# Optimization experiments

Hardware: AMD Instinct MI355X
Metric: run time of the kernel (lower is better)

The kernel has to match this reference:

```python
import jax, jax.numpy as jnp
import numpy as np

QUERY_SIZE = 512
KEY_SIZE = 512
VALUE_SIZE = 512
HIDDEN = 128


def setup_inputs() -> dict:
    key = jax.random.key(0)
    ks = jax.random.split(key, 9)
    b, t_q, t_k = 8, 128, 512
    query = jax.random.normal(ks[0], (b, t_q, QUERY_SIZE), dtype=jnp.float32)
    keys = jax.random.normal(ks[1], (b, t_k, KEY_SIZE), dtype=jnp.float32)
    values = jax.random.normal(ks[2], (b, t_k, VALUE_SIZE), dtype=jnp.float32)
    # torch nn.Linear init ~ U(-1/sqrt(fan_in), 1/sqrt(fan_in)); scale-matched normals are fine
    sq = 1.0 / np.sqrt(QUERY_SIZE)
    sk = 1.0 / np.sqrt(KEY_SIZE)
    sh = 1.0 / np.sqrt(HIDDEN)
    Wq = jax.random.uniform(ks[3], (HIDDEN, QUERY_SIZE), jnp.float32, -sq, sq)
    bq = jax.random.uniform(ks[4], (HIDDEN,), jnp.float32, -sq, sq)
    Wk = jax.random.uniform(ks[5], (HIDDEN, KEY_SIZE), jnp.float32, -sk, sk)
    bk = jax.random.uniform(ks[6], (HIDDEN,), jnp.float32, -sk, sk)
    Wo = jax.random.uniform(ks[7], (1, HIDDEN), jnp.float32, -sh, sh)
    bo = jax.random.uniform(ks[8], (1,), jnp.float32, -sh, sh)
    return {"query": query, "keys": keys, "values": values,
            "Wq": Wq, "bq": bq, "Wk": Wk, "bk": bk, "Wo": Wo, "bo": bo}


def reference(query, keys, values, Wq, bq, Wk, bk, Wo, bo):
    # Bahdanau additive attention: att_ij = Wo @ tanh(Wq q_i + Wk k_j + bq + bk) + bo
    # Project once per position (mathematically identical to the expanded per-pair Linear).
    q_proj = jnp.einsum('bqn,hn->bqh', query, Wq) + bq          # b x t_q x h
    k_proj = jnp.einsum('bkn,hn->bkh', keys, Wk) + bk           # b x t_k x h
    hid = jnp.tanh(q_proj[:, :, None, :] + k_proj[:, None, :, :])  # b x t_q x t_k x h
    scores = jnp.einsum('bqkh,h->bqk', hid, Wo[0]) + bo[0]       # b x t_q x t_k
    attn = jax.nn.softmax(scores, axis=2)
    context = jnp.einsum('bqk,bkv->bqv', attn, values)           # b x t_q x n_v
    return context, attn
```

## Files before the change

### kernel.cpp

```cpp
#include <hip/hip_runtime.h>


#define B_    8
#define TQ_   128
#define TK_   512
#define NIN_  512
#define H_    128
#define NV_   512
#define NQR   (B_*TQ_)
#define NROWS (NQR + B_*TK_)

#define C2_   2.8853900817779268f
#define L2E_  1.4426950408889634f

__device__ __forceinline__ float fexp2(float x){ return __builtin_amdgcn_exp2f(x); }
__device__ __forceinline__ float frcp (float x){ return __builtin_amdgcn_rcpf(x); }

__global__ __launch_bounds__(256, 5) void proj_kernel(
        const float* __restrict__ query, const float* __restrict__ keys,
        const float* __restrict__ Wq, const float* __restrict__ Wk,
        float* __restrict__ psum, int kper) {
    __shared__ float at[32][18];
    __shared__ float wt[32][132];
    const int tid = threadIdx.x;
    const int r0  = blockIdx.x * 16;
    const float* in; const float* W;
    if (r0 < NQR) { in = query + (size_t)r0 * NIN_;         W = Wq; }
    else          { in = keys  + (size_t)(r0 - NQR) * NIN_; W = Wk; }

    const int r2 = (tid >> 5) * 2;
    const int h4 = (tid & 31) * 4;
    const int ar  = tid >> 4;
    const int ak2 = (tid & 15) * 2;
    const int wr  = tid >> 3;
    const int wkq = (tid & 7) * 4;
    const int kb0 = blockIdx.y * kper;
    const int nc  = kper >> 5;

    const float* pA  = in + ar * NIN_ + kb0 + ak2;
    const float* pW0 = W + (wr     ) * NIN_ + kb0 + wkq;
    const float* pW1 = W + (wr + 32) * NIN_ + kb0 + wkq;
    const float* pW2 = W + (wr + 64) * NIN_ + kb0 + wkq;
    const float* pW3 = W + (wr + 96) * NIN_ + kb0 + wkq;

    float2 af  = *(const float2*)pA;
    float4 wf0 = *(const float4*)pW0;
    float4 wf1 = *(const float4*)pW1;
    float4 wf2 = *(const float4*)pW2;
    float4 wf3 = *(const float4*)pW3;

    float acc[2][4] = {{0.f,0.f,0.f,0.f},{0.f,0.f,0.f,0.f}};

    for (int c = 0; c < nc; ++c) {
        __syncthreads();
        at[ak2+0][ar] = af.x;  at[ak2+1][ar] = af.y;
        wt[wkq+0][wr   ] = wf0.x; wt[wkq+1][wr   ] = wf0.y;
        wt[wkq+2][wr   ] = wf0.z; wt[wkq+3][wr   ] = wf0.w;
        wt[wkq+0][wr+32] = wf1.x; wt[wkq+1][wr+32] = wf1.y;
        wt[wkq+2][wr+32] = wf1.z; wt[wkq+3][wr+32] = wf1.w;
        wt[wkq+0][wr+64] = wf2.x; wt[wkq+1][wr+64] = wf2.y;
        wt[wkq+2][wr+64] = wf2.z; wt[wkq+3][wr+64] = wf2.w;
        wt[wkq+0][wr+96] = wf3.x; wt[wkq+1][wr+96] = wf3.y;
        wt[wkq+2][wr+96] = wf3.z; wt[wkq+3][wr+96] = wf3.w;
        __syncthreads();
        if (c + 1 < nc) {
            pA += 32; pW0 += 32; pW1 += 32; pW2 += 32; pW3 += 32;
            af  = *(const float2*)pA;
            wf0 = *(const float4*)pW0; wf1 = *(const float4*)pW1;
            wf2 = *(const float4*)pW2; wf3 = *(const float4*)pW3;
        }
#pragma unroll 8
        for (int kk = 0; kk < 32; ++kk) {
            float2 a = *(const float2*)&at[kk][r2];
            float4 w = *(const float4*)&wt[kk][h4];
            acc[0][0] = fmaf(a.x, w.x, acc[0][0]);
            acc[0][1] = fmaf(a.x, w.y, acc[0][1]);
            acc[0][2] = fmaf(a.x, w.z, acc[0][2]);
            acc[0][3] = fmaf(a.x, w.w, acc[0][3]);
            acc[1][0] = fmaf(a.y, w.x, acc[1][0]);
            acc[1][1] = fmaf(a.y, w.y, acc[1][1]);
            acc[1][2] = fmaf(a.y, w.z, acc[1][2]);
            acc[1][3] = fmaf(a.y, w.w, acc[1][3]);
        }
    }

    float* op = psum + ((size_t)blockIdx.y * NROWS + r0) * H_;
#pragma unroll
    for (int i = 0; i < 2; ++i) {
        float4 o = {acc[i][0], acc[i][1], acc[i][2], acc[i][3]};
        *(float4*)&op[(r2 + i) * H_ + h4] = o;
    }
}

__global__ __launch_bounds__(256, 4) void reduce_kernel(
        const float* __restrict__ psum, const float* __restrict__ bq,
        const float* __restrict__ bk, float* __restrict__ pout) {
    const int i = blockIdx.x * 256 + threadIdx.x;
    const int row = i >> 5;
    const int h4  = (i & 31) * 4;
    const float* bias = (row < NQR) ? bq : bk;
    float4 s = *(const float4*)&bias[h4];
#pragma unroll
    for (int sp = 0; sp < 4; ++sp) {
        float4 p = *(const float4*)&psum[((size_t)sp * NROWS) * H_ + (size_t)i * 4];
        s.x += p.x; s.y += p.y; s.z += p.z; s.w += p.w;
    }
    *(float4*)&pout[(size_t)i * 4] = s;
}

__global__ __launch_bounds__(256, 4) void scores_kernel(
        const float* __restrict__ qp, const float* __restrict__ kp,
        const float* __restrict__ Wo, const float* __restrict__ bo,
        float* __restrict__ out_attn) {
    __shared__ float qs2[2][H_];
    __shared__ float w2[H_];
    __shared__ float sc[2][TK_];

    const int tid = threadIdx.x;
    const int b   = blockIdx.y;
    const int q0  = blockIdx.x * 2;
    const int lane = tid & 63;

    qs2[tid >> 7][tid & 127] =
        qp[(b * TQ_ + q0 + (tid >> 7)) * H_ + (tid & 127)] * C2_;
    if (tid < H_) w2[tid] = Wo[tid] * -2.0f;
    __syncthreads();

    float sw = w2[lane] + w2[lane + 64];
#pragma unroll
    for (int m = 1; m < 64; m <<= 1) sw += __shfl_xor(sw, m);
    const float sbase = bo[0] - 0.5f * sw;

#pragma unroll
    for (int half = 0; half < 2; ++half) {
        const int k = tid + half * 256;
        const float4* kp4 = (const float4*)&kp[(b * TK_ + k) * H_];
        float acc[2] = {0.f, 0.f};
#pragma unroll 4
        for (int hb = 0; hb < 32; ++hb) {
            float4 kv = kp4[hb];
            kv.x *= C2_; kv.y *= C2_; kv.z *= C2_; kv.w *= C2_;
            float4 wv = *(const float4*)&w2[hb * 4];
#pragma unroll
            for (int qi = 0; qi < 2; ++qi) {
                float4 qv = *(const float4*)&qs2[qi][hb * 4];
                float r0 = frcp(fexp2(qv.x + kv.x) + 1.0f);
                float r1 = frcp(fexp2(qv.y + kv.y) + 1.0f);
                float r2 = frcp(fexp2(qv.z + kv.z) + 1.0f);
                float r3 = frcp(fexp2(qv.w + kv.w) + 1.0f);
                acc[qi] = fmaf(wv.x, r0, acc[qi]);
                acc[qi] = fmaf(wv.y, r1, acc[qi]);
                acc[qi] = fmaf(wv.z, r2, acc[qi]);
                acc[qi] = fmaf(wv.w, r3, acc[qi]);
            }
        }
        sc[0][k] = acc[0] + sbase;
        sc[1][k] = acc[1] + sbase;
    }
    __syncthreads();

    const int w = tid >> 6;
    if (w < 2) {
        float4 sA = *(const float4*)&sc[w][lane * 8];
        float4 sB = *(const float4*)&sc[w][lane * 8 + 4];
        float m = fmaxf(fmaxf(fmaxf(sA.x, sA.y), fmaxf(sA.z, sA.w)),
                        fmaxf(fmaxf(sB.x, sB.y), fmaxf(sB.z, sB.w)));
#pragma unroll
        for (int mask = 1; mask < 64; mask <<= 1) m = fmaxf(m, __shfl_xor(m, mask));
        float4 eA, eB;
        eA.x = fexp2((sA.x - m) * L2E_); eA.y = fexp2((sA.y - m) * L2E_);
        eA.z = fexp2((sA.z - m) * L2E_); eA.w = fexp2((sA.w - m) * L2E_);
        eB.x = fexp2((sB.x - m) * L2E_); eB.y = fexp2((sB.y - m) * L2E_);
        eB.z = fexp2((sB.z - m) * L2E_); eB.w = fexp2((sB.w - m) * L2E_);
        float s = eA.x + eA.y + eA.z + eA.w + eB.x + eB.y + eB.z + eB.w;
#pragma unroll
        for (int mask = 1; mask < 64; mask <<= 1) s += __shfl_xor(s, mask);
        float inv = frcp(s);
        eA.x *= inv; eA.y *= inv; eA.z *= inv; eA.w *= inv;
        eB.x *= inv; eB.y *= inv; eB.z *= inv; eB.w *= inv;
        float4* op = (float4*)&out_attn[(b * TQ_ + q0 + w) * TK_ + lane * 8];
        op[0] = eA; op[1] = eB;
    }
}

__global__ __launch_bounds__(256, 4) void context_kernel(
        const float* __restrict__ attn, const float* __restrict__ values,
        float* __restrict__ outc) {
    __shared__ float at[32][20];
    __shared__ float vt[32][132];

    const int tid = threadIdx.x;
    const int b   = blockIdx.y;
    const int q0  = (blockIdx.x >> 2) * 16;
    const int v0  = (blockIdx.x & 3) * 128;

    const int tx = tid & 31, ty = tid >> 5;
    const int v4 = tx * 4,   r2 = ty * 2;
    const int ar = tid >> 3, akq = (tid & 7) * 4;
    const int vk = tid >> 5;

    const float* pAt = attn + (size_t)(b * TQ_ + q0 + ar) * TK_ + akq;
    const float* pV0 = values + (size_t)(b * TK_ + vk     ) * NV_ + v0 + v4;
    const float* pV1 = values + (size_t)(b * TK_ + vk +  8) * NV_ + v0 + v4;
    const float* pV2 = values + (size_t)(b * TK_ + vk + 16) * NV_ + v0 + v4;
    const float* pV3 = values + (size_t)(b * TK_ + vk + 24) * NV_ + v0 + v4;

    float4 af = {0.f,0.f,0.f,0.f};
    if (tid < 128) af = *(const float4*)pAt;
    float4 vf0 = *(const float4*)pV0;
    float4 vf1 = *(const float4*)pV1;
    float4 vf2 = *(const float4*)pV2;
    float4 vf3 = *(const float4*)pV3;

    float acc[2][4] = {{0.f,0.f,0.f,0.f},{0.f,0.f,0.f,0.f}};

    for (int c = 0; c < 16; ++c) {
        __syncthreads();
        if (tid < 128) {
            at[akq+0][ar] = af.x; at[akq+1][ar] = af.y;
            at[akq+2][ar] = af.z; at[akq+3][ar] = af.w;
        }
        *(float4*)&vt[vk     ][v4] = vf0;
        *(float4*)&vt[vk +  8][v4] = vf1;
        *(float4*)&vt[vk + 16][v4] = vf2;
        *(float4*)&vt[vk + 24][v4] = vf3;
        __syncthreads();
        if (c + 1 < 16) {
            pAt += 32; pV0 += 32 * NV_; pV1 += 32 * NV_;
            pV2 += 32 * NV_; pV3 += 32 * NV_;
            if (tid < 128) af = *(const float4*)pAt;
            vf0 = *(const float4*)pV0; vf1 = *(const float4*)pV1;
            vf2 = *(const float4*)pV2; vf3 = *(const float4*)pV3;
        }
#pragma unroll 8
        for (int kk = 0; kk < 32; ++kk) {
            float2 a = *(const float2*)&at[kk][r2];
            float4 v = *(const float4*)&vt[kk][v4];
            acc[0][0] = fmaf(a.x, v.x, acc[0][0]);
            acc[0][1] = fmaf(a.x, v.y, acc[0][1]);
            acc[0][2] = fmaf(a.x, v.z, acc[0][2]);
            acc[0][3] = fmaf(a.x, v.w, acc[0][3]);
            acc[1][0] = fmaf(a.y, v.x, acc[1][0]);
            acc[1][1] = fmaf(a.y, v.y, acc[1][1]);
            acc[1][2] = fmaf(a.y, v.z, acc[1][2]);
            acc[1][3] = fmaf(a.y, v.w, acc[1][3]);
        }
    }
    float4 o0 = {acc[0][0], acc[0][1], acc[0][2], acc[0][3]};
    float4 o1 = {acc[1][0], acc[1][1], acc[1][2], acc[1][3]};
    *(float4*)&outc[(size_t)(b * TQ_ + q0 + r2 + 0) * NV_ + v0 + v4] = o0;
    *(float4*)&outc[(size_t)(b * TQ_ + q0 + r2 + 1) * NV_ + v0 + v4] = o1;
}

extern "C" void kernel_launch(void* const* d_in, const int* in_sizes, int n_in,
                              void* d_out, int out_size, void* d_ws, size_t ws_size,
                              hipStream_t stream) {
    const float* query  = (const float*)d_in[0];
    const float* keys   = (const float*)d_in[1];
    const float* values = (const float*)d_in[2];
    const float* Wq     = (const float*)d_in[3];
    const float* bq     = (const float*)d_in[4];
    const float* Wk     = (const float*)d_in[5];
    const float* bk     = (const float*)d_in[6];
    const float* Wo     = (const float*)d_in[7];
    const float* bo     = (const float*)d_in[8];

    float* out_ctx  = (float*)d_out;
    float* out_attn = out_ctx + B_ * TQ_ * NV_;
    float* proj_out = (float*)d_ws;
    float* qp = proj_out;
    float* kp = proj_out + NQR * H_;
    float* psum = proj_out + NROWS * H_;

    proj_kernel<<<dim3(NROWS / 16, 4), 256, 0, stream>>>(
        query, keys, Wq, Wk, psum, NIN_ / 4);
    reduce_kernel<<<(NROWS * H_ / 4) / 256, 256, 0, stream>>>(
        psum, bq, bk, proj_out);
    scores_kernel<<<dim3(TQ_ / 2, B_), 256, 0, stream>>>(qp, kp, Wo, bo, out_attn);
    context_kernel<<<dim3(32, B_), 256, 0, stream>>>(out_attn, values, out_ctx);
}
```

Measured before the change: 68.61 us.

## Store key projections transposed and pre-scaled for coalesced scores-kernel loads

The reduce kernel now writes the key projections transposed (b, h, k) through an LDS tile and pre-multiplies them by the tanh scaling constant. The scores kernel then has each thread handle four consecutive keys for one query and walk over h, so its loads are coalesced float4 reads across threads, where before each thread strided through a whole 512-byte row. This also drops the per-element C2 multiply from the inner loop. The cost is an LDS transpose and a block-wide barrier in the reduce kernel.

After: 68.92 us. Within noise of the previous version (+0.4%).

```diff
diff --git a/kernel.cpp b/kernel.cpp
--- a/kernel.cpp
+++ b/kernel.cpp
@@ -94,22 +94,48 @@
 
 __global__ __launch_bounds__(256, 4) void reduce_kernel(
         const float* __restrict__ psum, const float* __restrict__ bq,
-        const float* __restrict__ bk, float* __restrict__ pout) {
-    const int i = blockIdx.x * 256 + threadIdx.x;
-    const int row = i >> 5;
-    const int h4  = (i & 31) * 4;
-    const float* bias = (row < NQR) ? bq : bk;
-    float4 s = *(const float4*)&bias[h4];
-#pragma unroll
-    for (int sp = 0; sp < 4; ++sp) {
-        float4 p = *(const float4*)&psum[((size_t)sp * NROWS) * H_ + (size_t)i * 4];
-        s.x += p.x; s.y += p.y; s.z += p.z; s.w += p.w;
-    }
-    *(float4*)&pout[(size_t)i * 4] = s;
+        const float* __restrict__ bk, float* __restrict__ qp,
+        float* __restrict__ kpT) {
+    __shared__ float lt[128][17];
+    const int tid = threadIdx.x;
+    const int r0  = blockIdx.x * 16;
+    const bool isq = (r0 < NQR);
+    const float* bias = isq ? bq : bk;
+
+#pragma unroll
+    for (int p = 0; p < 2; ++p) {
+        const int j = tid + p * 256;
+        const int row = j >> 5, hq = (j & 31) * 4;
+        const float4 b4 = *(const float4*)&bias[hq];
+        float4 s = b4;
+#pragma unroll
+        for (int sp = 0; sp < 4; ++sp) {
+            float4 v = *(const float4*)&psum[((size_t)sp * NROWS + r0 + row) * H_ + hq];
+            s.x += v.x; s.y += v.y; s.z += v.z; s.w += v.w;
+        }
+        if (isq) {
+            *(float4*)&qp[(size_t)(r0 + row) * H_ + hq] = s;
+        } else {
+            lt[hq + 0][row] = s.x * C2_; lt[hq + 1][row] = s.y * C2_;
+            lt[hq + 2][row] = s.z * C2_; lt[hq + 3][row] = s.w * C2_;
+        }
+    }
+    if (!isq) {
+        __syncthreads();
+        const int b  = (r0 - NQR) >> 9;
+        const int k0 = (r0 - NQR) & 511;
+#pragma unroll
+        for (int p = 0; p < 2; ++p) {
+            const int j = tid + p * 256;
+            const int h = j >> 2, kq = (j & 3) * 4;
+            float4 o = {lt[h][kq], lt[h][kq + 1], lt[h][kq + 2], lt[h][kq + 3]};
+            *(float4*)&kpT[((size_t)b * H_ + h) * TK_ + k0 + kq] = o;
+        }
+    }
 }
 
 __global__ __launch_bounds__(256, 4) void scores_kernel(
-        const float* __restrict__ qp, const float* __restrict__ kp,
+        const float* __restrict__ qp, const float* __restrict__ kpT,
         const float* __restrict__ Wo, const float* __restrict__ bo,
         float* __restrict__ out_attn) {
     __shared__ float qs2[2][H_];
@@ -131,32 +157,23 @@
     for (int m = 1; m < 64; m <<= 1) sw += __shfl_xor(sw, m);
     const float sbase = bo[0] - 0.5f * sw;
 
-#pragma unroll
-    for (int half = 0; half < 2; ++half) {
-        const int k = tid + half * 256;
-        const float4* kp4 = (const float4*)&kp[(b * TK_ + k) * H_];
-        float acc[2] = {0.f, 0.f};
+    const int k4 = (tid & 127) * 4;
+    const int qi = tid >> 7;
+    const float* pk = kpT + (size_t)b * H_ * TK_ + k4;
+    float a0 = 0.f, a1 = 0.f, a2 = 0.f, a3 = 0.f;
 #pragma unroll 4
-        for (int hb = 0; hb < 32; ++hb) {
-            float4 kv = kp4[hb];
-            kv.x *= C2_; kv.y *= C2_; kv.z *= C2_; kv.w *= C2_;
-            float4 wv = *(const float4*)&w2[hb * 4];
-#pragma unroll
-            for (int qi = 0; qi < 2; ++qi) {
-                float4 qv = *(const float4*)&qs2[qi][hb * 4];
-                float r0 = frcp(fexp2(qv.x + kv.x) + 1.0f);
-                float r1 = frcp(fexp2(qv.y + kv.y) + 1.0f);
-                float r2 = frcp(fexp2(qv.z + kv.z) + 1.0f);
-                float r3 = frcp(fexp2(qv.w + kv.w) + 1.0f);
-                acc[qi] = fmaf(wv.x, r0, acc[qi]);
-                acc[qi] = fmaf(wv.y, r1, acc[qi]);
-                acc[qi] = fmaf(wv.z, r2, acc[qi]);
-                acc[qi] = fmaf(wv.w, r3, acc[qi]);
-            }
-        }
-        sc[0][k] = acc[0] + sbase;
-        sc[1][k] = acc[1] + sbase;
-    }
+    for (int h = 0; h < H_; ++h) {
+        float4 kv = *(const float4*)pk;
+        pk += TK_;
+        const float qv = qs2[qi][h];
+        const float wv = w2[h];
+        a0 = fmaf(wv, frcp(fexp2(qv + kv.x) + 1.0f), a0);
+        a1 = fmaf(wv, frcp(fexp2(qv + kv.y) + 1.0f), a1);
+        a2 = fmaf(wv, frcp(fexp2(qv + kv.z) + 1.0f), a2);
+        a3 = fmaf(wv, frcp(fexp2(qv + kv.w) + 1.0f), a3);
+    }
+    float4 sv = {a0 + sbase, a1 + sbase, a2 + sbase, a3 + sbase};
+    *(float4*)&sc[qi][k4] = sv;
     __syncthreads();
 
     const int w = tid >> 6;
@@ -267,15 +284,13 @@
 
     float* out_ctx  = (float*)d_out;
     float* out_attn = out_ctx + B_ * TQ_ * NV_;
-    float* proj_out = (float*)d_ws;
-    float* qp = proj_out;
-    float* kp = proj_out + NQR * H_;
-    float* psum = proj_out + NROWS * H_;
+    float* qp   = (float*)d_ws;
+    float* kpT  = qp + (size_t)NQR * H_;
+    float* psum = kpT + (size_t)B_ * H_ * TK_;
 
     proj_kernel<<<dim3(NROWS / 16, 4), 256, 0, stream>>>(
         query, keys, Wq, Wk, psum, NIN_ / 4);
-    reduce_kernel<<<(NROWS * H_ / 4) / 256, 256, 0, stream>>>(
-        psum, bq, bk, proj_out);
-    scores_kernel<<<dim3(TQ_ / 2, B_), 256, 0, stream>>>(qp, kp, Wo, bo, out_attn);
+    reduce_kernel<<<NROWS / 16, 256, 0, stream>>>(psum, bq, bk, qp, kpT);
+    scores_kernel<<<dim3(TQ_ / 2, B_), 256, 0, stream>>>(qp, kpT, Wo, bo, out_attn);
     context_kernel<<<dim3(32, B_), 256, 0, stream>>>(out_attn, values, out_ctx);
 }
```
